# Optimization experiments

Hardware: AMD Instinct MI355X
Metric: run time of the kernel (lower is better)

Reference implementation:

```python
import jax, jax.numpy as jnp
import numpy as np

N = 50000          # nodes
E_RAND = 1_600_000 # random edges (avg degree 32)
IN = 8             # in_features
OUT = 8            # out_features
B = 16             # batch columns of x
T = 5              # edge types AFTER add_self_loops (type 1 = self loop, 2..5 = original)


def setup_inputs() -> dict:
    key = jax.random.key(0)
    k1, k2, k3, k4, k5, k6 = jax.random.split(key, 6)
    x = jax.random.normal(k1, (N * IN, B), jnp.float32)
    loops = jnp.arange(N, dtype=jnp.int32)
    # self loops prepended (type 1), random edges with types 2..T (original types shifted +1)
    src = jnp.concatenate([loops, jax.random.randint(k2, (E_RAND,), 0, N, jnp.int32)])
    dst = jnp.concatenate([loops, jax.random.randint(k3, (E_RAND,), 0, N, jnp.int32)])
    edge_types = jnp.concatenate([
        jnp.ones(N, jnp.int32),
        jax.random.randint(k4, (E_RAND,), 2, T + 1, jnp.int32),
    ])
    bound = 1.0 / np.sqrt(IN)
    # weight_vector reshaped: expand() maps ext_type = ((e-1)*OUT + i)*IN + j + 1
    W = jax.random.uniform(k5, (T, OUT, IN), jnp.float32, -bound, bound)
    # bias_vector reshaped: expand(OUT, 1) -> per (type, out-row) scalar
    Bv = jax.random.uniform(k6, (T, OUT), jnp.float32, -bound, bound)
    return dict(x=x, W=W, Bv=Bv, src=src, dst=dst, edge_types=edge_types)


def reference(x, W, Bv, src, dst, edge_types):
    T_, OUT_, IN_ = W.shape
    Nn = x.shape[0] // IN_
    xr = x.reshape(Nn, IN_, -1)                 # [N, in, B]
    Wg = W[edge_types - 1]                      # [E, out, in] per-edge weight block gather
    msg = jnp.einsum('eoi,eib->eob', Wg, xr[src])  # [E, out, B]
    y = jax.ops.segment_sum(msg, dst, num_segments=Nn)            # [N, out, B]
    yb = jax.ops.segment_sum(Bv[edge_types - 1], dst, num_segments=Nn)  # [N, out]
    y = y + yb[:, :, None]
    return y.reshape(Nn * OUT_, -1)             # [N*out, B]
```

## Files before the change

kernel.cpp:

```cpp
#include <hip/hip_runtime.h>
#include <hip/hip_fp16.h>

#define N_NODES 50000
#define E_RAND  1600000
#define IN_F    8
#define OUT_F   8
#define BATCH   16

#define NB      391
#define CAP     4608
#define OSTRIDE 513
#define CHUNK   6144
#define BIN_BLOCKS  ((E_RAND + CHUNK - 1) / CHUNK)
#define CONV_BLOCKS 1563

#define OFF_BCUR   0
#define OFF_OFF    2048
#define OFF_XH     804864
#define OFF_BINNED 13604864
#define OFF_SORTED 20811776
#define WS_NEEDED  28018688

__global__ __launch_bounds__(512)
void zero_kernel(int* __restrict__ p, int n) {
    const int i = blockIdx.x * 512 + threadIdx.x;
    if (i < n) p[i] = 0;
}

__global__ __launch_bounds__(512)
void prep_kernel(const float* __restrict__ x, __half* __restrict__ xh,
                 const int* __restrict__ src, const int* __restrict__ dst,
                 const int* __restrict__ et,
                 int* __restrict__ bcur, int* __restrict__ binned) {
    if (blockIdx.x < CONV_BLOCKS) {
        const int b = threadIdx.x & 15;
        const int n = blockIdx.x * 32 + (threadIdx.x >> 4);
        if (n >= N_NODES) return;
        const float* xp = x + n * (IN_F * BATCH) + b;
        union { __half h[8]; uint4 u; } pk;
#pragma unroll
        for (int i = 0; i < IN_F; ++i) pk.h[i] = __float2half(xp[i * BATCH]);
        *(uint4*)(xh + (size_t)n * 128 + b * 8) = pk.u;
        return;
    }
    __shared__ int h[NB];
    __shared__ int rbase[NB];
    for (int i = threadIdx.x; i < NB; i += 512) h[i] = 0;
    __syncthreads();
    const int cbase = (blockIdx.x - CONV_BLOCKS) * CHUNK;
#pragma unroll 4
    for (int k = 0; k < CHUNK / 512; ++k) {
        const int e = cbase + k * 512 + threadIdx.x;
        if (e < E_RAND) atomicAdd(&h[dst[N_NODES + e] >> 7], 1);
    }
    __syncthreads();
    for (int i = threadIdx.x; i < NB; i += 512) {
        const int c = h[i];
        rbase[i] = c ? atomicAdd(&bcur[i], c) : 0;
        h[i] = 0;
    }
    __syncthreads();
#pragma unroll 4
    for (int k = 0; k < CHUNK / 512; ++k) {
        const int e = cbase + k * 512 + threadIdx.x;
        if (e < E_RAND) {
            const int ee  = N_NODES + e;
            const int d   = dst[ee];
            const int bkt = d >> 7;
            const int payload = ((((d & 127) << 2) | (et[ee] - 2)) << 16) | src[ee];
            binned[bkt * CAP + rbase[bkt] + atomicAdd(&h[bkt], 1)] = payload;
        }
    }
}

__global__ __launch_bounds__(512)
void bucket_sort(const int* __restrict__ bcur, const int* __restrict__ binned,
                 int* __restrict__ off, int* __restrict__ sorted) {
    __shared__ int h[512];
    __shared__ int wtot[8];
    const int bkt  = blockIdx.x;
    const int cnt  = bcur[bkt];
    const int base = bkt * CAP;
    const int t = threadIdx.x;
    h[t] = 0;
    __syncthreads();
    for (int i = t; i < cnt; i += 512)
        atomicAdd(&h[binned[base + i] >> 16], 1);
    __syncthreads();
    const int v = h[t];
    const int lane = t & 63, wid = t >> 6;
    int inc = v;
#pragma unroll
    for (int d = 1; d < 64; d <<= 1) {
        const int u = __shfl_up(inc, d);
        if (lane >= d) inc += u;
    }
    if (lane == 63) wtot[wid] = inc;
    __syncthreads();
    int wbase = 0;
    for (int w = 0; w < wid; ++w) wbase += wtot[w];
    const int start = base + wbase + inc - v;
    h[t] = start;
    off[bkt * OSTRIDE + t] = start;
    if (t == 511) off[bkt * OSTRIDE + 512] = base + cnt;
    __syncthreads();
    for (int i = t; i < cnt; i += 512) {
        const int p = binned[base + i];
        sorted[atomicAdd(&h[p >> 16], 1)] = p & 0xFFFF;
    }
}

__device__ __forceinline__ void unpack_add(uint4 v, float* xa) {
    const __half2* hp = (const __half2*)&v;
    float2 f;
    f = __half22float2(hp[0]); xa[0] += f.x; xa[1] += f.y;
    f = __half22float2(hp[1]); xa[2] += f.x; xa[3] += f.y;
    f = __half22float2(hp[2]); xa[4] += f.x; xa[5] += f.y;
    f = __half22float2(hp[3]); xa[6] += f.x; xa[7] += f.y;
}

__global__ __launch_bounds__(256)
void gather_kernel(const __half* __restrict__ xh,
                   const float* __restrict__ W,
                   const float* __restrict__ Bv,
                   const int* __restrict__ off,
                   const int* __restrict__ sidx,
                   float* __restrict__ y) {
    const int lane = threadIdx.x & 63;
    const int n = blockIdx.x * 4 + (threadIdx.x >> 6);
    const int g = lane >> 4;
    const int b = lane & 15;
    const int o0 = g * 2;
    const int boff = b * 8;

    float out[2];
    {
        float xs[IN_F];
#pragma unroll
        for (int i = 0; i < IN_F; ++i) xs[i] = 0.f;
        unpack_add(*(const uint4*)(xh + (size_t)n * 128 + boff), xs);
#pragma unroll
        for (int c = 0; c < 2; ++c) {
            const int o = o0 + c;
            const float4 w0 = ((const float4*)(W + o * IN_F))[0];
            const float4 w1 = ((const float4*)(W + o * IN_F))[1];
            float a = Bv[o];
            a = fmaf(w0.x, xs[0], a); a = fmaf(w0.y, xs[1], a);
            a = fmaf(w0.z, xs[2], a); a = fmaf(w0.w, xs[3], a);
            a = fmaf(w1.x, xs[4], a); a = fmaf(w1.y, xs[5], a);
            a = fmaf(w1.z, xs[6], a); a = fmaf(w1.w, xs[7], a);
            out[c] = a;
        }
    }

    const int* offp = off + 4 * n + (n >> 7);
    int so[5];
#pragma unroll
    for (int j = 0; j < 5; ++j) so[j] = offp[j];

#pragma unroll
    for (int t = 0; t < 4; ++t) {
        const int s0 = so[t];
        const int s1 = so[t + 1];
        const int cnt = s1 - s0;
        if (cnt == 0) continue;
        const int last = s1 - 1;

        float xa[IN_F];
#pragma unroll
        for (int i = 0; i < IN_F; ++i) xa[i] = 0.f;

        int e    = s0 + g;
        int srcA = sidx[min(e, last)];
        int srcB = sidx[min(e + 4, last)];
        uint4 rowA = *(const uint4*)(xh + (size_t)srcA * 128 + boff);
        while (e < s1) {
            const uint4 rowB = *(const uint4*)(xh + (size_t)srcB * 128 + boff);
            const int  srcC  = sidx[min(e + 8, last)];
            unpack_add(rowA, xa);
            rowA = rowB; srcB = srcC; e += 4;
        }

#pragma unroll
        for (int i = 0; i < IN_F; ++i) {
            xa[i] += __shfl_xor(xa[i], 16);
            xa[i] += __shfl_xor(xa[i], 32);
        }

        const float* Wt = W + (t + 1) * (OUT_F * IN_F);
        const float* Bt = Bv + (t + 1) * OUT_F;
        const float fc = (float)cnt;
#pragma unroll
        for (int c = 0; c < 2; ++c) {
            const int o = o0 + c;
            const float4 w0 = ((const float4*)(Wt + o * IN_F))[0];
            const float4 w1 = ((const float4*)(Wt + o * IN_F))[1];
            float a = fmaf(fc, Bt[o], out[c]);
            a = fmaf(w0.x, xa[0], a); a = fmaf(w0.y, xa[1], a);
            a = fmaf(w0.z, xa[2], a); a = fmaf(w0.w, xa[3], a);
            a = fmaf(w1.x, xa[4], a); a = fmaf(w1.y, xa[5], a);
            a = fmaf(w1.z, xa[6], a); a = fmaf(w1.w, xa[7], a);
            out[c] = a;
        }
    }

    float* yp = y + n * (OUT_F * BATCH) + b;
    yp[(o0    ) * BATCH] = out[0];
    yp[(o0 + 1) * BATCH] = out[1];
}

__global__ __launch_bounds__(256)
void selfinit_kernel(const float* __restrict__ x,
                     const float* __restrict__ W,
                     const float* __restrict__ Bv,
                     float* __restrict__ y) {
    const int b = threadIdx.x & (BATCH - 1);
    const int n = blockIdx.x * 16 + (threadIdx.x >> 4);
    if (n >= N_NODES) return;
    float xc[IN_F];
#pragma unroll
    for (int i = 0; i < IN_F; ++i) xc[i] = x[(n * IN_F + i) * BATCH + b];
#pragma unroll
    for (int o = 0; o < OUT_F; ++o) {
        float a = Bv[o];
#pragma unroll
        for (int i = 0; i < IN_F; ++i) a = fmaf(W[o * IN_F + i], xc[i], a);
        y[(n * OUT_F + o) * BATCH + b] = a;
    }
}

__global__ __launch_bounds__(256)
void direct_edge_kernel(const float* __restrict__ x,
                        const float* __restrict__ W,
                        const float* __restrict__ Bv,
                        const int* __restrict__ src,
                        const int* __restrict__ dst,
                        const int* __restrict__ et,
                        float* __restrict__ y) {
    const int tid = blockIdx.x * 256 + threadIdx.x;
    const int eg  = tid >> 4;
    const int b   = tid & (BATCH - 1);
    if (eg >= E_RAND) return;
    const int e  = N_NODES + eg;
    const int s  = src[e];
    const int d  = dst[e];
    const int ti = et[e] - 1;
    const float* __restrict__ Wt = W + ti * (OUT_F * IN_F);
    float xc[IN_F];
#pragma unroll
    for (int i = 0; i < IN_F; ++i) xc[i] = x[(s * IN_F + i) * BATCH + b];
    float* yp = y + (size_t)d * (OUT_F * BATCH) + b;
#pragma unroll
    for (int o = 0; o < OUT_F; ++o) {
        float a = Bv[ti * OUT_F + o];
#pragma unroll
        for (int i = 0; i < IN_F; ++i) a = fmaf(Wt[o * IN_F + i], xc[i], a);
        unsafeAtomicAdd(yp + o * BATCH, a);
    }
}

extern "C" void kernel_launch(void* const* d_in, const int* in_sizes, int n_in,
                              void* d_out, int out_size, void* d_ws, size_t ws_size,
                              hipStream_t stream) {
    const float* x   = (const float*)d_in[0];
    const float* W   = (const float*)d_in[1];
    const float* Bv  = (const float*)d_in[2];
    const int*   src = (const int*)d_in[3];
    const int*   dst = (const int*)d_in[4];
    const int*   et  = (const int*)d_in[5];
    float* y = (float*)d_out;

    char* ws = (char*)d_ws;
    int*    bcur   = (int*)(ws + OFF_BCUR);
    int*    off    = (int*)(ws + OFF_OFF);
    __half* xh     = (__half*)(ws + OFF_XH);
    int*    binned = (int*)(ws + OFF_BINNED);
    int*    sorted = (int*)(ws + OFF_SORTED);

    if (ws_size >= WS_NEEDED) {
        zero_kernel<<<1, 512, 0, stream>>>(bcur, NB);
        prep_kernel<<<CONV_BLOCKS + BIN_BLOCKS, 512, 0, stream>>>(x, xh, src, dst, et, bcur, binned);
        bucket_sort<<<NB, 512, 0, stream>>>(bcur, binned, off, sorted);
        gather_kernel<<<N_NODES / 4, 256, 0, stream>>>(xh, W, Bv, off, sorted, y);
    } else {
        selfinit_kernel<<<(N_NODES + 15) / 16, 256, 0, stream>>>(x, W, Bv, y);
        direct_edge_kernel<<<(E_RAND * 16 + 255) / 256, 256, 0, stream>>>(x, W, Bv, src, dst, et, y);
    }
}
```

Before: 209.1 us.

## Fuse bucket sort and gather into one kernel with LDS-resident sorted indices

Merges the per-bucket counting sort and the gather/aggregate into a single kernel. Bucket size is halved to 64 destination nodes so the sorted source list fits in shared memory, which removes the global sorted/offset arrays and one launch. W and Bv are staged in LDS, and each 16-lane group now handles all 8 outputs for a node by walking edges serially, replacing the previous split of edges across 4 groups with shuffle reductions. The trade-off is only 782 blocks of 512 threads, heavy LDS use per block, and a gather loop with less memory-level parallelism and no prefetch, which could limit latency hiding.

```diff
diff --git a/kernel.cpp b/kernel.cpp
--- a/kernel.cpp
+++ b/kernel.cpp
@@ -6,20 +6,18 @@
 #define IN_F    8
 #define OUT_F   8
 #define BATCH   16
-
-#define NB      391
-#define CAP     4608
-#define OSTRIDE 513
+#define T_TYPES 5
+
+#define NB      782
+#define CAP     2432
 #define CHUNK   6144
 #define BIN_BLOCKS  ((E_RAND + CHUNK - 1) / CHUNK)
 #define CONV_BLOCKS 1563
 
 #define OFF_BCUR   0
-#define OFF_OFF    2048
-#define OFF_XH     804864
-#define OFF_BINNED 13604864
-#define OFF_SORTED 20811776
-#define WS_NEEDED  28018688
+#define OFF_XH     4096
+#define OFF_BINNED 12804096
+#define WS_NEEDED  (OFF_BINNED + (size_t)NB * CAP * 4)
 
 __global__ __launch_bounds__(512)
 void zero_kernel(int* __restrict__ p, int n) {
@@ -51,7 +49,7 @@
 #pragma unroll 4
     for (int k = 0; k < CHUNK / 512; ++k) {
         const int e = cbase + k * 512 + threadIdx.x;
-        if (e < E_RAND) atomicAdd(&h[dst[N_NODES + e] >> 7], 1);
+        if (e < E_RAND) atomicAdd(&h[dst[N_NODES + e] >> 6], 1);
     }
     __syncthreads();
     for (int i = threadIdx.x; i < NB; i += 512) {
@@ -66,47 +64,10 @@
         if (e < E_RAND) {
             const int ee  = N_NODES + e;
             const int d   = dst[ee];
-            const int bkt = d >> 7;
-            const int payload = ((((d & 127) << 2) | (et[ee] - 2)) << 16) | src[ee];
+            const int bkt = d >> 6;
+            const int payload = ((((d & 63) << 2) | (et[ee] - 2)) << 16) | src[ee];
             binned[bkt * CAP + rbase[bkt] + atomicAdd(&h[bkt], 1)] = payload;
         }
-    }
-}
-
-__global__ __launch_bounds__(512)
-void bucket_sort(const int* __restrict__ bcur, const int* __restrict__ binned,
-                 int* __restrict__ off, int* __restrict__ sorted) {
-    __shared__ int h[512];
-    __shared__ int wtot[8];
-    const int bkt  = blockIdx.x;
-    const int cnt  = bcur[bkt];
-    const int base = bkt * CAP;
-    const int t = threadIdx.x;
-    h[t] = 0;
-    __syncthreads();
-    for (int i = t; i < cnt; i += 512)
-        atomicAdd(&h[binned[base + i] >> 16], 1);
-    __syncthreads();
-    const int v = h[t];
-    const int lane = t & 63, wid = t >> 6;
-    int inc = v;
-#pragma unroll
-    for (int d = 1; d < 64; d <<= 1) {
-        const int u = __shfl_up(inc, d);
-        if (lane >= d) inc += u;
-    }
-    if (lane == 63) wtot[wid] = inc;
-    __syncthreads();
-    int wbase = 0;
-    for (int w = 0; w < wid; ++w) wbase += wtot[w];
-    const int start = base + wbase + inc - v;
-    h[t] = start;
-    off[bkt * OSTRIDE + t] = start;
-    if (t == 511) off[bkt * OSTRIDE + 512] = base + cnt;
-    __syncthreads();
-    for (int i = t; i < cnt; i += 512) {
-        const int p = binned[base + i];
-        sorted[atomicAdd(&h[p >> 16], 1)] = p & 0xFFFF;
     }
 }
 
@@ -119,94 +80,130 @@
     f = __half22float2(hp[3]); xa[6] += f.x; xa[7] += f.y;
 }
 
-__global__ __launch_bounds__(256)
-void gather_kernel(const __half* __restrict__ xh,
-                   const float* __restrict__ W,
-                   const float* __restrict__ Bv,
-                   const int* __restrict__ off,
-                   const int* __restrict__ sidx,
-                   float* __restrict__ y) {
-    const int lane = threadIdx.x & 63;
-    const int n = blockIdx.x * 4 + (threadIdx.x >> 6);
-    const int g = lane >> 4;
-    const int b = lane & 15;
-    const int o0 = g * 2;
+__global__ __launch_bounds__(512)
+void sortgather_kernel(const __half* __restrict__ xh,
+                       const float* __restrict__ W,
+                       const float* __restrict__ Bv,
+                       const int* __restrict__ bcur,
+                       const int* __restrict__ binned,
+                       float* __restrict__ y) {
+    __shared__ int   lsort[CAP];
+    __shared__ int   hist[256];
+    __shared__ int   cur[256];
+    __shared__ int   segoff[257];
+    __shared__ float Wl[T_TYPES * OUT_F * IN_F];
+    __shared__ float Bvl[T_TYPES * OUT_F];
+    __shared__ int   wtot[4];
+
+    const int bkt  = blockIdx.x;
+    const int cnt  = bcur[bkt];
+    const int base = bkt * CAP;
+    const int t    = threadIdx.x;
+
+    if (t < 320) Wl[t] = W[t];
+    if (t >= 384 && t < 424) Bvl[t - 384] = Bv[t - 384];
+    if (t < 256) hist[t] = 0;
+    __syncthreads();
+
+    for (int i = t; i < cnt; i += 512)
+        atomicAdd(&hist[binned[base + i] >> 16], 1);
+    __syncthreads();
+
+    if (t < 256) {
+        const int lane = t & 63;
+        int inc = hist[t];
+#pragma unroll
+        for (int d = 1; d < 64; d <<= 1) {
+            const int u = __shfl_up(inc, d);
+            if (lane >= d) inc += u;
+        }
+        cur[t] = inc;
+        if (lane == 63) wtot[t >> 6] = inc;
+    }
+    __syncthreads();
+    if (t < 256) {
+        const int wv = t >> 6;
+        int wbase = 0;
+        for (int w = 0; w < wv; ++w) wbase += wtot[w];
+        const int excl = wbase + cur[t] - hist[t];
+        segoff[t] = excl;
+        cur[t]    = excl;
+        if (t == 255) segoff[256] = cnt;
+    }
+    __syncthreads();
+
+    for (int i = t; i < cnt; i += 512) {
+        const int p = binned[base + i];
+        lsort[atomicAdd(&cur[p >> 16], 1)] = p & 0xFFFF;
+    }
+    __syncthreads();
+
+    const int gg   = t >> 4;
+    const int b    = t & 15;
     const int boff = b * 8;
 
-    float out[2];
-    {
+#pragma unroll
+    for (int half = 0; half < 2; ++half) {
+        const int ln = gg + half * 32;
+        const int n  = bkt * 64 + ln;
+        if (n >= N_NODES) continue;
+
         float xs[IN_F];
 #pragma unroll
         for (int i = 0; i < IN_F; ++i) xs[i] = 0.f;
         unpack_add(*(const uint4*)(xh + (size_t)n * 128 + boff), xs);
-#pragma unroll
-        for (int c = 0; c < 2; ++c) {
-            const int o = o0 + c;
-            const float4 w0 = ((const float4*)(W + o * IN_F))[0];
-            const float4 w1 = ((const float4*)(W + o * IN_F))[1];
-            float a = Bv[o];
+
+        float out[OUT_F];
+#pragma unroll
+        for (int o = 0; o < OUT_F; ++o) {
+            const float4 w0 = ((const float4*)(Wl + o * IN_F))[0];
+            const float4 w1 = ((const float4*)(Wl + o * IN_F))[1];
+            float a = Bvl[o];
             a = fmaf(w0.x, xs[0], a); a = fmaf(w0.y, xs[1], a);
             a = fmaf(w0.z, xs[2], a); a = fmaf(w0.w, xs[3], a);
             a = fmaf(w1.x, xs[4], a); a = fmaf(w1.y, xs[5], a);
             a = fmaf(w1.z, xs[6], a); a = fmaf(w1.w, xs[7], a);
-            out[c] = a;
-        }
-    }
-
-    const int* offp = off + 4 * n + (n >> 7);
-    int so[5];
-#pragma unroll
-    for (int j = 0; j < 5; ++j) so[j] = offp[j];
-
-#pragma unroll
-    for (int t = 0; t < 4; ++t) {
-        const int s0 = so[t];
-        const int s1 = so[t + 1];
-        const int cnt = s1 - s0;
-        if (cnt == 0) continue;
-        const int last = s1 - 1;
-
-        float xa[IN_F];
-#pragma unroll
-        for (int i = 0; i < IN_F; ++i) xa[i] = 0.f;
-
-        int e    = s0 + g;
-        int srcA = sidx[min(e, last)];
-        int srcB = sidx[min(e + 4, last)];
-        uint4 rowA = *(const uint4*)(xh + (size_t)srcA * 128 + boff);
-        while (e < s1) {
-            const uint4 rowB = *(const uint4*)(xh + (size_t)srcB * 128 + boff);
-            const int  srcC  = sidx[min(e + 8, last)];
-            unpack_add(rowA, xa);
-            rowA = rowB; srcB = srcC; e += 4;
-        }
-
-#pragma unroll
-        for (int i = 0; i < IN_F; ++i) {
-            xa[i] += __shfl_xor(xa[i], 16);
-            xa[i] += __shfl_xor(xa[i], 32);
-        }
-
-        const float* Wt = W + (t + 1) * (OUT_F * IN_F);
-        const float* Bt = Bv + (t + 1) * OUT_F;
-        const float fc = (float)cnt;
-#pragma unroll
-        for (int c = 0; c < 2; ++c) {
-            const int o = o0 + c;
-            const float4 w0 = ((const float4*)(Wt + o * IN_F))[0];
-            const float4 w1 = ((const float4*)(Wt + o * IN_F))[1];
-            float a = fmaf(fc, Bt[o], out[c]);
-            a = fmaf(w0.x, xa[0], a); a = fmaf(w0.y, xa[1], a);
-            a = fmaf(w0.z, xa[2], a); a = fmaf(w0.w, xa[3], a);
-            a = fmaf(w1.x, xa[4], a); a = fmaf(w1.y, xa[5], a);
-            a = fmaf(w1.z, xa[6], a); a = fmaf(w1.w, xa[7], a);
-            out[c] = a;
-        }
-    }
-
-    float* yp = y + n * (OUT_F * BATCH) + b;
-    yp[(o0    ) * BATCH] = out[0];
-    yp[(o0 + 1) * BATCH] = out[1];
+            out[o] = a;
+        }
+
+        const int* sp = segoff + ln * 4;
+#pragma unroll
+        for (int t4 = 0; t4 < 4; ++t4) {
+            const int s0 = sp[t4];
+            const int s1 = sp[t4 + 1];
+            const int c  = s1 - s0;
+            if (c == 0) continue;
+
+            float xa[IN_F];
+#pragma unroll
+            for (int i = 0; i < IN_F; ++i) xa[i] = 0.f;
+
+            for (int e = s0; e < s1; ++e) {
+                const int src = lsort[e];
+                unpack_add(*(const uint4*)(xh + (size_t)src * 128 + boff), xa);
+            }
+
+            const float* Wt = Wl + (t4 + 1) * (OUT_F * IN_F);
+            const float* Bt = Bvl + (t4 + 1) * OUT_F;
+            const float fc = (float)c;
+#pragma unroll
+            for (int o = 0; o < OUT_F; ++o) {
+                const float4 w0 = ((const float4*)(Wt + o * IN_F))[0];
+                const float4 w1 = ((const float4*)(Wt + o * IN_F))[1];
+                float a = fmaf(fc, Bt[o], out[o]);
+                a = fmaf(w0.x, xa[0], a); a = fmaf(w0.y, xa[1], a);
+                a = fmaf(w0.z, xa[2], a); a = fmaf(w0.w, xa[3], a);
+                a = fmaf(w1.x, xa[4], a); a = fmaf(w1.y, xa[5], a);
+                a = fmaf(w1.z, xa[6], a); a = fmaf(w1.w, xa[7], a);
+                out[o] = a;
+            }
+        }
+
+        float* yp = y + (size_t)n * (OUT_F * BATCH) + b;
+#pragma unroll
+        for (int o = 0; o < OUT_F; ++o)
+            yp[o * BATCH] = out[o];
+    }
 }
 
 __global__ __launch_bounds__(256)
@@ -272,16 +269,13 @@
 
     char* ws = (char*)d_ws;
     int*    bcur   = (int*)(ws + OFF_BCUR);
-    int*    off    = (int*)(ws + OFF_OFF);
     __half* xh     = (__half*)(ws + OFF_XH);
     int*    binned = (int*)(ws + OFF_BINNED);
-    int*    sorted = (int*)(ws + OFF_SORTED);
 
     if (ws_size >= WS_NEEDED) {
-        zero_kernel<<<1, 512, 0, stream>>>(bcur, NB);
+        zero_kernel<<<2, 512, 0, stream>>>(bcur, NB);
         prep_kernel<<<CONV_BLOCKS + BIN_BLOCKS, 512, 0, stream>>>(x, xh, src, dst, et, bcur, binned);
-        bucket_sort<<<NB, 512, 0, stream>>>(bcur, binned, off, sorted);
-        gather_kernel<<<N_NODES / 4, 256, 0, stream>>>(xh, W, Bv, off, sorted, y);
+        sortgather_kernel<<<NB, 512, 0, stream>>>(xh, W, Bv, bcur, binned, y);
     } else {
         selfinit_kernel<<<(N_NODES + 15) / 16, 256, 0, stream>>>(x, W, Bv, y);
         direct_edge_kernel<<<(E_RAND * 16 + 255) / 256, 256, 0, stream>>>(x, W, Bv, src, dst, et, y);
```

New measurement: 186.6 us. -10.8%, faster.
